# Optimization experiments

Hardware: AMD Instinct MI355X
Metric: run time of the kernel (lower is better)

Reference implementation:

```python
import jax, jax.numpy as jnp
from jax import lax
import numpy as np


def setup_inputs() -> dict:
    key = jax.random.key(0)
    ks = jax.random.split(key, 5)
    B, T, I, H, L = 64, 512, 1024, 1024, 1
    stdv = 1.0 / (H ** 0.5)
    return {
        "input": jax.random.normal(ks[0], (B, T, I), dtype=jnp.float32),
        "weight_ih": jax.random.uniform(ks[1], (L, H, I), jnp.float32, -stdv, stdv),
        "weight_hh": jax.random.uniform(ks[2], (L, H, H), jnp.float32, -stdv, stdv),
        "bias_ih": jax.random.uniform(ks[3], (L, H), jnp.float32, -stdv, stdv),
        "bias_hh": jax.random.uniform(ks[4], (L, H), jnp.float32, -stdv, stdv),
    }


def reference(input, weight_ih, weight_hh, bias_ih, bias_hh):
    # input: (B, T, I); weights per layer; hx: (L, B, H)
    L, H, I = weight_ih.shape
    B, T, _ = input.shape
    h0 = jnp.zeros((L, B, H), dtype=input.dtype)
    bias = (bias_ih + bias_hh)[:, None, :]  # (L, 1, H)
    # Hoist the input projection out of the recurrence: one big GEMM.
    x_proj = jnp.einsum("bti,lhi->tlbh", input, weight_ih)  # (T, L, B, H)

    def step(h, xp):
        # h: (L, B, H); per-layer recurrent matmul
        g = xp + jnp.einsum("lbh,lgh->lbg", h, weight_hh) + bias
        h_new = jnp.tanh(g)
        return h_new, h_new

    h_last, outs = lax.scan(step, h0, x_proj)  # outs: (T, L, B, H)
    output = jnp.transpose(outs, (1, 0, 2, 3))  # (L, T, B, H) matching torch cat(dim=1)
    return output, h_last
```

## Files before the change

kernel.cpp:

```cpp
#include <hip/hip_runtime.h>
#include <hip/hip_bf16.h>
#include <stdint.h>

#define B_ 64
#define T_ 512
#define I_ 1024
#define H_ 1024
#define BH (B_*H_)

typedef __attribute__((ext_vector_type(8))) short short8;
typedef __attribute__((ext_vector_type(4))) float f32x4;
typedef __attribute__((ext_vector_type(4))) unsigned u32x4;
typedef __attribute__((ext_vector_type(2))) unsigned u32x2;

static __device__ __forceinline__ unsigned short f2bf(float f) {
  union { float f; unsigned u; } v; v.f = f;
  unsigned r = v.u + 0x7fffu + ((v.u >> 16) & 1u);
  return (unsigned short)(r >> 16);
}

static __device__ __forceinline__ void glds16(const void* g, void* l) {
  __builtin_amdgcn_global_load_lds(
      (const __attribute__((address_space(1))) unsigned int*)g,
      (__attribute__((address_space(3))) unsigned int*)l, 16, 0, 0);
}

__global__ void convert_weights(const f32x4* __restrict__ wih, const f32x4* __restrict__ whh,
                                uint2* __restrict__ wih_b, uint2* __restrict__ whh_b)
{
  int idx = blockIdx.x * blockDim.x + threadIdx.x;
  f32x4 a = wih[idx];
  uint2 o;
  o.x = f2bf(a[0]) | ((unsigned)f2bf(a[1]) << 16);
  o.y = f2bf(a[2]) | ((unsigned)f2bf(a[3]) << 16);
  wih_b[idx] = o;
  f32x4 b = whh[idx];
  uint2 p;
  p.x = f2bf(b[0]) | ((unsigned)f2bf(b[1]) << 16);
  p.y = f2bf(b[2]) | ((unsigned)f2bf(b[3]) << 16);
  whh_b[idx] = p;
}

__global__ void convert_input(const float* __restrict__ in, unsigned short* __restrict__ inb)
{
  size_t idx = (size_t)blockIdx.x * 256 + threadIdx.x;
  size_t base = idx * 8;
  size_t R = base >> 10;
  int i = (int)(base & 1023);
  int b = (int)(R & 63), t = (int)(R >> 6);
  const float* src = in + ((size_t)b * T_ + (size_t)t) * I_ + i;
  f32x4 x0 = *(const f32x4*)src;
  f32x4 x1 = *(const f32x4*)(src + 4);
  uint4 o;
  o.x = f2bf(x0[0]) | ((unsigned)f2bf(x0[1]) << 16);
  o.y = f2bf(x0[2]) | ((unsigned)f2bf(x0[3]) << 16);
  o.z = f2bf(x1[0]) | ((unsigned)f2bf(x1[1]) << 16);
  o.w = f2bf(x1[2]) | ((unsigned)f2bf(x1[3]) << 16);
  *(uint4*)(inb + base) = o;
}

__launch_bounds__(256)
__global__ void gemm_xproj(const unsigned short* __restrict__ inb,
                           const unsigned short* __restrict__ wb,
                           const float* __restrict__ bih,
                           const float* __restrict__ bhh,
                           float* __restrict__ out)
{
  __shared__ __align__(16) unsigned char As[16384];
  __shared__ __align__(16) unsigned char Bs[16384];
  const int tid = threadIdx.x;
  const int lane = tid & 63;
  const int w = tid >> 6;
  const int wm = w >> 1, wn = w & 1;
  const int bn = blockIdx.x, bm = blockIdx.y;

  f32x4 acc[4][4];
  #pragma unroll
  for (int i = 0; i < 4; ++i)
    #pragma unroll
    for (int j = 0; j < 4; ++j)
      acc[i][j] = (f32x4){0.f,0.f,0.f,0.f};

  for (int kt = 0; kt < 16; ++kt) {
    __syncthreads();
    #pragma unroll
    for (int q = 0; q < 4; ++q) {
      int inst = w*4 + q;
      int rr = inst*8 + (lane >> 3);
      int soA = ((bm*128 + rr) * I_ + kt*64) * 2 + (((lane & 7) * 16) ^ ((rr & 7) << 4));
      int soB = ((bn*128 + rr) * I_ + kt*64) * 2 + (((lane & 7) * 16) ^ ((rr & 7) << 4));
      glds16((const unsigned char*)inb + soA, As + inst*1024);
      glds16((const unsigned char*)wb  + soB, Bs + inst*1024);
    }
    __syncthreads();
    #pragma unroll
    for (int kb = 0; kb < 2; ++kb) {
      const int kby = kb*64 + ((lane >> 4) << 4);
      short8 af[4], bfr[4];
      #pragma unroll
      for (int i = 0; i < 4; ++i) {
        int ra = wm*64 + i*16 + (lane & 15);
        af[i] = *(const short8*)(As + ra*128 + (kby ^ ((ra & 7) << 4)));
      }
      #pragma unroll
      for (int j = 0; j < 4; ++j) {
        int rb2 = wn*64 + j*16 + (lane & 15);
        bfr[j] = *(const short8*)(Bs + rb2*128 + (kby ^ ((rb2 & 7) << 4)));
      }
      #pragma unroll
      for (int i = 0; i < 4; ++i)
        #pragma unroll
        for (int j = 0; j < 4; ++j)
          acc[i][j] = __builtin_amdgcn_mfma_f32_16x16x32_bf16(af[i], bfr[j], acc[i][j], 0, 0, 0);
    }
  }
  #pragma unroll
  for (int j = 0; j < 4; ++j) {
    int col = bn*128 + wn*64 + j*16 + (lane & 15);
    float bias = bih[col] + bhh[col];
    #pragma unroll
    for (int i = 0; i < 4; ++i) {
      int Rb = bm*128 + wm*64 + i*16 + ((lane >> 4) << 2);
      #pragma unroll
      for (int q = 0; q < 4; ++q) {
        int R = Rb + q;
        out[(size_t)(R >> 6) * BH + (size_t)(R & 63) * H_ + col] = acc[i][j][q] + bias;
      }
    }
  }
}

__launch_bounds__(256, 1)
__global__ void rnn_recur(const unsigned short* __restrict__ whh_b,
                          float* __restrict__ out,
                          unsigned char* __restrict__ hx)
{
  extern __shared__ __align__(16) unsigned char lds[];
  const int tid = threadIdx.x;
  const int lane = tid & 63;
  const int w = tid >> 6;
  const int g = blockIdx.x;
  const int gb = g >> 4;
  const int gn = g & 15;

  for (int q = 0; q < 32; ++q) {
    int inst = w*32 + q;
    int nl = inst >> 1;
    int koff = (inst & 1)*1024 + lane*16;
    size_t srcoff = (size_t)(gn*64 + nl)*2048 + (size_t)(koff ^ ((nl & 7) << 4));
    glds16((const unsigned char*)whh_b + srcoff, lds + inst*1024);
  }
  asm volatile("s_waitcnt vmcnt(0)" ::: "memory");
  __syncthreads();

  const int arow = w*16 + (lane & 15);
  const unsigned char* wsrow = lds + (size_t)arow*2048;
  const int aswz = (arow & 7) << 4;
  const int klane = (lane >> 4) << 4;
  short8 af[32];
  #pragma unroll
  for (int kb = 0; kb < 32; ++kb)
    af[kb] = *(const short8*)(wsrow + ((kb*64 + klane) ^ aswz));
  __syncthreads();

  const int bb = lane & 15;
  const int nq = (lane >> 4) << 2;
  const int colb = gn*64 + w*16 + nq;
  const int brow = gb*16 + bb;
  const int bswz = (bb & 7) << 4;

  const int srow = tid & 15;
  const int scol = tid >> 4;
  const int sswz = (srow & 7) << 4;

  f32x4 xp = *(const f32x4*)(out + (size_t)brow*H_ + colb);

  for (int t = 0; t < T_; ++t) {
    unsigned char* hsb = lds + (size_t)(t & 1)*32768;
    unsigned char* sdst = hsb + srow*2048;
    if (t == 0) {
      u32x2 z = (u32x2){0u, 0u};
      #pragma unroll
      for (int j = 0; j < 16; ++j)
        *(u32x2*)(sdst + (((j*16 + scol)*8) ^ sswz)) = z;
    } else {
      const unsigned want = (unsigned)t;
      const unsigned char* pb = hx + (size_t)(t & 1)*262144 + (size_t)gb*65536 + (size_t)tid*16;
      u32x4 v0,v1,v2,v3,v4,v5,v6,v7,v8,v9,v10,v11,v12,v13,v14,v15;
      __builtin_amdgcn_s_sleep(8);
      asm volatile(
        "global_load_dwordx4 %0, %8, off sc0 sc1\n\t"
        "global_load_dwordx4 %1, %9, off sc0 sc1\n\t"
        "global_load_dwordx4 %2, %10, off sc0 sc1\n\t"
        "global_load_dwordx4 %3, %11, off sc0 sc1\n\t"
        "global_load_dwordx4 %4, %12, off sc0 sc1\n\t"
        "global_load_dwordx4 %5, %13, off sc0 sc1\n\t"
        "global_load_dwordx4 %6, %14, off sc0 sc1\n\t"
        "global_load_dwordx4 %7, %15, off sc0 sc1"
        : "=&v"(v0),"=&v"(v1),"=&v"(v2),"=&v"(v3),"=&v"(v4),"=&v"(v5),"=&v"(v6),"=&v"(v7)
        : "v"(pb), "v"(pb+4096), "v"(pb+2*4096), "v"(pb+3*4096),
          "v"(pb+4*4096), "v"(pb+5*4096), "v"(pb+6*4096), "v"(pb+7*4096)
        : "memory");
      asm volatile(
        "global_load_dwordx4 %0, %8, off sc0 sc1\n\t"
        "global_load_dwordx4 %1, %9, off sc0 sc1\n\t"
        "global_load_dwordx4 %2, %10, off sc0 sc1\n\t"
        "global_load_dwordx4 %3, %11, off sc0 sc1\n\t"
        "global_load_dwordx4 %4, %12, off sc0 sc1\n\t"
        "global_load_dwordx4 %5, %13, off sc0 sc1\n\t"
        "global_load_dwordx4 %6, %14, off sc0 sc1\n\t"
        "global_load_dwordx4 %7, %15, off sc0 sc1"
        : "=&v"(v8),"=&v"(v9),"=&v"(v10),"=&v"(v11),"=&v"(v12),"=&v"(v13),"=&v"(v14),"=&v"(v15)
        : "v"(pb+8*4096), "v"(pb+9*4096), "v"(pb+10*4096), "v"(pb+11*4096),
          "v"(pb+12*4096), "v"(pb+13*4096), "v"(pb+14*4096), "v"(pb+15*4096)
        : "memory");
      asm volatile("s_waitcnt vmcnt(0)"
        : "+v"(v0),"+v"(v1),"+v"(v2),"+v"(v3),"+v"(v4),"+v"(v5),"+v"(v6),"+v"(v7),
          "+v"(v8),"+v"(v9),"+v"(v10),"+v"(v11),"+v"(v12),"+v"(v13),"+v"(v14),"+v"(v15)
        :: "memory");
      unsigned m;
      #define MKMASK() { m = 0; \
        m |= (v0[2]==want)  ? 1u<<0  : 0u;  m |= (v1[2]==want)  ? 1u<<1  : 0u; \
        m |= (v2[2]==want)  ? 1u<<2  : 0u;  m |= (v3[2]==want)  ? 1u<<3  : 0u; \
        m |= (v4[2]==want)  ? 1u<<4  : 0u;  m |= (v5[2]==want)  ? 1u<<5  : 0u; \
        m |= (v6[2]==want)  ? 1u<<6  : 0u;  m |= (v7[2]==want)  ? 1u<<7  : 0u; \
        m |= (v8[2]==want)  ? 1u<<8  : 0u;  m |= (v9[2]==want)  ? 1u<<9  : 0u; \
        m |= (v10[2]==want) ? 1u<<10 : 0u;  m |= (v11[2]==want) ? 1u<<11 : 0u; \
        m |= (v12[2]==want) ? 1u<<12 : 0u;  m |= (v13[2]==want) ? 1u<<13 : 0u; \
        m |= (v14[2]==want) ? 1u<<14 : 0u;  m |= (v15[2]==want) ? 1u<<15 : 0u; }
      MKMASK()
      while (m != 0xffffu) {
        __builtin_amdgcn_s_sleep(1);
        #define RLD(vv, jj) if (!((m >> (jj)) & 1u)) \
          asm volatile("global_load_dwordx4 %0, %1, off sc0 sc1" \
                       : "=&v"(vv) : "v"(pb + (jj)*4096) : "memory");
        RLD(v0,0)  RLD(v1,1)  RLD(v2,2)  RLD(v3,3)
        RLD(v4,4)  RLD(v5,5)  RLD(v6,6)  RLD(v7,7)
        RLD(v8,8)  RLD(v9,9)  RLD(v10,10) RLD(v11,11)
        RLD(v12,12) RLD(v13,13) RLD(v14,14) RLD(v15,15)
        #undef RLD
        asm volatile("s_waitcnt vmcnt(0)"
          : "+v"(v0),"+v"(v1),"+v"(v2),"+v"(v3),"+v"(v4),"+v"(v5),"+v"(v6),"+v"(v7),
            "+v"(v8),"+v"(v9),"+v"(v10),"+v"(v11),"+v"(v12),"+v"(v13),"+v"(v14),"+v"(v15)
          :: "memory");
        MKMASK()
      }
      #undef MKMASK
      #define STG(vv, jj) \
        *(u32x2*)(sdst + ((((jj)*16 + scol)*8) ^ sswz)) = (u32x2){vv[0], vv[1]};
      STG(v0,0)  STG(v1,1)  STG(v2,2)  STG(v3,3)
      STG(v4,4)  STG(v5,5)  STG(v6,6)  STG(v7,7)
      STG(v8,8)  STG(v9,9)  STG(v10,10) STG(v11,11)
      STG(v12,12) STG(v13,13) STG(v14,14) STG(v15,15)
      #undef STG
    }
    asm volatile("s_waitcnt lgkmcnt(0)\n\ts_barrier" ::: "memory");

    const unsigned char* hfrow = hsb + (size_t)bb*2048;
    f32x4 acc0 = (f32x4){0.f,0.f,0.f,0.f}, acc1 = acc0, acc2 = acc0, acc3 = acc0;
    #pragma unroll
    for (int kb = 0; kb < 32; kb += 4) {
      short8 b0 = *(const short8*)(hfrow + ((kb*64 + klane) ^ bswz));
      short8 b1 = *(const short8*)(hfrow + (((kb+1)*64 + klane) ^ bswz));
      short8 b2 = *(const short8*)(hfrow + (((kb+2)*64 + klane) ^ bswz));
      short8 b3 = *(const short8*)(hfrow + (((kb+3)*64 + klane) ^ bswz));
      acc0 = __builtin_amdgcn_mfma_f32_16x16x32_bf16(af[kb],   b0, acc0, 0, 0, 0);
      acc1 = __builtin_amdgcn_mfma_f32_16x16x32_bf16(af[kb+1], b1, acc1, 0, 0, 0);
      acc2 = __builtin_amdgcn_mfma_f32_16x16x32_bf16(af[kb+2], b2, acc2, 0, 0, 0);
      acc3 = __builtin_amdgcn_mfma_f32_16x16x32_bf16(af[kb+3], b3, acc3, 0, 0, 0);
    }
    f32x4 hval;
    #pragma unroll
    for (int q = 0; q < 4; ++q)
      hval[q] = tanhf((acc0[q] + acc1[q]) + (acc2[q] + acc3[q]) + xp[q]);

    u32x4 pkt;
    pkt[0] = f2bf(hval[0]) | ((unsigned)f2bf(hval[1]) << 16);
    pkt[1] = f2bf(hval[2]) | ((unsigned)f2bf(hval[3]) << 16);
    pkt[2] = (unsigned)(t + 1);
    pkt[3] = 0u;
    const unsigned char* wp = hx + (size_t)((t+1) & 1)*262144 + (size_t)gb*65536
                              + (size_t)(gn*256 + tid)*16;
    asm volatile("global_store_dwordx4 %0, %1, off sc0 sc1" :: "v"(wp), "v"(pkt) : "memory");

    *(f32x4*)(out + (size_t)t*BH + (size_t)brow*H_ + colb) = hval;
    if (t == T_-1)
      *(f32x4*)(out + (size_t)T_*BH + (size_t)brow*H_ + colb) = hval;

    int tn = (t < T_-1) ? t+1 : t;
    xp = *(const f32x4*)(out + (size_t)tn*BH + (size_t)brow*H_ + colb);
  }
}

extern "C" void kernel_launch(void* const* d_in, const int* in_sizes, int n_in,
                              void* d_out, int out_size, void* d_ws, size_t ws_size,
                              hipStream_t stream)
{
  const float* in  = (const float*)d_in[0];
  const float* wih = (const float*)d_in[1];
  const float* whh = (const float*)d_in[2];
  const float* bih = (const float*)d_in[3];
  const float* bhh = (const float*)d_in[4];
  float* out = (float*)d_out;
  unsigned char* ws = (unsigned char*)d_ws;

  unsigned char*  hx    = ws;
  unsigned short* wih_b = (unsigned short*)(ws + 524288);
  unsigned short* whh_b = (unsigned short*)(ws + 524288 + 2097152);
  unsigned short* inb   = (unsigned short*)(ws + 524288 + 4194304);

  hipMemsetAsync(hx, 0, 524288, stream);
  convert_weights<<<1024, 256, 0, stream>>>((const f32x4*)wih, (const f32x4*)whh,
                                            (uint2*)wih_b, (uint2*)whh_b);
  convert_input<<<16384, 256, 0, stream>>>(in, inb);
  gemm_xproj<<<dim3(8, 256), 256, 0, stream>>>(inb, whh_b == 0 ? 0 : wih_b, bih, bhh, out);
  rnn_recur<<<64, 256, 131072, stream>>>(whh_b, out, hx);
}
```

Baseline: 1.556 ms.

## Fuse input-projection GEMM with recurrence using per-row-block completion flags

Merges the fp32-to-bf16 input conversion into the GEMM's A-tile loader and runs the GEMM and the recurrence in a single launch. The first 64 blocks do the recurrence and the other 2048 blocks compute x_proj tiles. Each GEMM tile bumps an atomic flag per row-block, and a recurrent step spins on that flag before it reads x_proj, so the recurrence can start before the whole GEMM finishes. This removes a separate conversion pass and the kernel boundary. The risks are that the persistent recurrent blocks must be resident alongside the GEMM blocks, which a 128KB LDS request per block may limit, and that the x_proj reads now go uncached through sc0 sc1 loads.

```diff
diff --git a/kernel.cpp b/kernel.cpp
--- a/kernel.cpp
+++ b/kernel.cpp
@@ -41,104 +41,115 @@
   whh_b[idx] = p;
 }
 
-__global__ void convert_input(const float* __restrict__ in, unsigned short* __restrict__ inb)
+__launch_bounds__(256, 1)
+__global__ void fused_gemm_rnn(const float* __restrict__ in,
+                               const unsigned short* __restrict__ wih_b,
+                               const unsigned short* __restrict__ whh_b,
+                               const float* __restrict__ bih,
+                               const float* __restrict__ bhh,
+                               float* __restrict__ out,
+                               unsigned char* __restrict__ hx)
 {
-  size_t idx = (size_t)blockIdx.x * 256 + threadIdx.x;
-  size_t base = idx * 8;
-  size_t R = base >> 10;
-  int i = (int)(base & 1023);
-  int b = (int)(R & 63), t = (int)(R >> 6);
-  const float* src = in + ((size_t)b * T_ + (size_t)t) * I_ + i;
-  f32x4 x0 = *(const f32x4*)src;
-  f32x4 x1 = *(const f32x4*)(src + 4);
-  uint4 o;
-  o.x = f2bf(x0[0]) | ((unsigned)f2bf(x0[1]) << 16);
-  o.y = f2bf(x0[2]) | ((unsigned)f2bf(x0[3]) << 16);
-  o.z = f2bf(x1[0]) | ((unsigned)f2bf(x1[1]) << 16);
-  o.w = f2bf(x1[2]) | ((unsigned)f2bf(x1[3]) << 16);
-  *(uint4*)(inb + base) = o;
-}
-
-__launch_bounds__(256)
-__global__ void gemm_xproj(const unsigned short* __restrict__ inb,
-                           const unsigned short* __restrict__ wb,
-                           const float* __restrict__ bih,
-                           const float* __restrict__ bhh,
-                           float* __restrict__ out)
-{
-  __shared__ __align__(16) unsigned char As[16384];
-  __shared__ __align__(16) unsigned char Bs[16384];
+  extern __shared__ __align__(16) unsigned char lds[];
+  unsigned* flags = (unsigned*)(hx + 524288);
   const int tid = threadIdx.x;
   const int lane = tid & 63;
   const int w = tid >> 6;
-  const int wm = w >> 1, wn = w & 1;
-  const int bn = blockIdx.x, bm = blockIdx.y;
-
-  f32x4 acc[4][4];
-  #pragma unroll
-  for (int i = 0; i < 4; ++i)
-    #pragma unroll
-    for (int j = 0; j < 4; ++j)
-      acc[i][j] = (f32x4){0.f,0.f,0.f,0.f};
-
-  for (int kt = 0; kt < 16; ++kt) {
+
+  if (blockIdx.x >= 64) {
+    const int idx = blockIdx.x - 64;
+    const int bn = idx & 7;
+    const int bm = idx >> 3;
+    unsigned char* As = lds;
+    unsigned char* Bs = lds + 16384;
+    const int wm_ = w >> 1, wn = w & 1;
+
+    const int ar = tid >> 1;
+    const int ah = tid & 1;
+    const int R0 = bm*128 + ar;
+    const float* asrc = in + (size_t)(R0 & 63) * (T_*I_) + (size_t)(R0 >> 6) * I_ + ah*32;
+    unsigned char* adst_base = As + ar*128;
+    const int aswz_w = (ar & 7) << 4;
+
+    f32x4 acc[4][4];
+    #pragma unroll
+    for (int i = 0; i < 4; ++i)
+      #pragma unroll
+      for (int j = 0; j < 4; ++j)
+        acc[i][j] = (f32x4){0.f,0.f,0.f,0.f};
+
+    f32x4 av[8];
+    #pragma unroll
+    for (int j = 0; j < 8; ++j) av[j] = *(const f32x4*)(asrc + 0*64 + j*4);
+
+    for (int kt = 0; kt < 16; ++kt) {
+      __syncthreads();
+      #pragma unroll
+      for (int q = 0; q < 4; ++q) {
+        int inst = w*4 + q;
+        int rb = inst*8 + (lane >> 3);
+        int srcoff = ((bn*128 + rb) * I_ + kt*64) * 2 + (((lane & 7) * 16) ^ ((rb & 7) << 4));
+        glds16((const unsigned char*)wih_b + srcoff, Bs + inst*1024);
+      }
+      #pragma unroll
+      for (int j2 = 0; j2 < 4; ++j2) {
+        uint4 val;
+        f32x4 v0 = av[j2*2], v1 = av[j2*2+1];
+        val.x = f2bf(v0[0]) | ((unsigned)f2bf(v0[1]) << 16);
+        val.y = f2bf(v0[2]) | ((unsigned)f2bf(v0[3]) << 16);
+        val.z = f2bf(v1[0]) | ((unsigned)f2bf(v1[1]) << 16);
+        val.w = f2bf(v1[2]) | ((unsigned)f2bf(v1[3]) << 16);
+        int koffb = ah*64 + j2*16;
+        *(uint4*)(adst_base + (koffb ^ aswz_w)) = val;
+      }
+      __syncthreads();
+      if (kt < 15) {
+        #pragma unroll
+        for (int j = 0; j < 8; ++j) av[j] = *(const f32x4*)(asrc + (kt+1)*64 + j*4);
+      }
+      #pragma unroll
+      for (int kb = 0; kb < 2; ++kb) {
+        const int kby = kb*64 + ((lane >> 4) << 4);
+        short8 af2[4], bfr[4];
+        #pragma unroll
+        for (int i = 0; i < 4; ++i) {
+          int ra = wm_*64 + i*16 + (lane & 15);
+          af2[i] = *(const short8*)(As + ra*128 + (kby ^ ((ra & 7) << 4)));
+        }
+        #pragma unroll
+        for (int j = 0; j < 4; ++j) {
+          int rb2 = wn*64 + j*16 + (lane & 15);
+          bfr[j] = *(const short8*)(Bs + rb2*128 + (kby ^ ((rb2 & 7) << 4)));
+        }
+        #pragma unroll
+        for (int i = 0; i < 4; ++i)
+          #pragma unroll
+          for (int j = 0; j < 4; ++j)
+            acc[i][j] = __builtin_amdgcn_mfma_f32_16x16x32_bf16(af2[i], bfr[j], acc[i][j], 0, 0, 0);
+      }
+    }
+    #pragma unroll
+    for (int j = 0; j < 4; ++j) {
+      int col = bn*128 + wn*64 + j*16 + (lane & 15);
+      float bias = bih[col] + bhh[col];
+      #pragma unroll
+      for (int i = 0; i < 4; ++i) {
+        int Rb = bm*128 + wm_*64 + i*16 + ((lane >> 4) << 2);
+        #pragma unroll
+        for (int q = 0; q < 4; ++q) {
+          int R = Rb + q;
+          float vv = acc[i][j][q] + bias;
+          const float* addr = out + (size_t)(R >> 6) * BH + (size_t)(R & 63) * H_ + col;
+          asm volatile("global_store_dword %0, %1, off sc0 sc1" :: "v"(addr), "v"(vv) : "memory");
+        }
+      }
+    }
+    asm volatile("s_waitcnt vmcnt(0)" ::: "memory");
     __syncthreads();
-    #pragma unroll
-    for (int q = 0; q < 4; ++q) {
-      int inst = w*4 + q;
-      int rr = inst*8 + (lane >> 3);
-      int soA = ((bm*128 + rr) * I_ + kt*64) * 2 + (((lane & 7) * 16) ^ ((rr & 7) << 4));
-      int soB = ((bn*128 + rr) * I_ + kt*64) * 2 + (((lane & 7) * 16) ^ ((rr & 7) << 4));
-      glds16((const unsigned char*)inb + soA, As + inst*1024);
-      glds16((const unsigned char*)wb  + soB, Bs + inst*1024);
-    }
-    __syncthreads();
-    #pragma unroll
-    for (int kb = 0; kb < 2; ++kb) {
-      const int kby = kb*64 + ((lane >> 4) << 4);
-      short8 af[4], bfr[4];
-      #pragma unroll
-      for (int i = 0; i < 4; ++i) {
-        int ra = wm*64 + i*16 + (lane & 15);
-        af[i] = *(const short8*)(As + ra*128 + (kby ^ ((ra & 7) << 4)));
-      }
-      #pragma unroll
-      for (int j = 0; j < 4; ++j) {
-        int rb2 = wn*64 + j*16 + (lane & 15);
-        bfr[j] = *(const short8*)(Bs + rb2*128 + (kby ^ ((rb2 & 7) << 4)));
-      }
-      #pragma unroll
-      for (int i = 0; i < 4; ++i)
-        #pragma unroll
-        for (int j = 0; j < 4; ++j)
-          acc[i][j] = __builtin_amdgcn_mfma_f32_16x16x32_bf16(af[i], bfr[j], acc[i][j], 0, 0, 0);
-    }
+    if (tid == 0) atomicAdd(flags + bm, 1u);
+    return;
   }
-  #pragma unroll
-  for (int j = 0; j < 4; ++j) {
-    int col = bn*128 + wn*64 + j*16 + (lane & 15);
-    float bias = bih[col] + bhh[col];
-    #pragma unroll
-    for (int i = 0; i < 4; ++i) {
-      int Rb = bm*128 + wm*64 + i*16 + ((lane >> 4) << 2);
-      #pragma unroll
-      for (int q = 0; q < 4; ++q) {
-        int R = Rb + q;
-        out[(size_t)(R >> 6) * BH + (size_t)(R & 63) * H_ + col] = acc[i][j][q] + bias;
-      }
-    }
-  }
-}
-
-__launch_bounds__(256, 1)
-__global__ void rnn_recur(const unsigned short* __restrict__ whh_b,
-                          float* __restrict__ out,
-                          unsigned char* __restrict__ hx)
-{
-  extern __shared__ __align__(16) unsigned char lds[];
-  const int tid = threadIdx.x;
-  const int lane = tid & 63;
-  const int w = tid >> 6;
+
   const int g = blockIdx.x;
   const int gb = g >> 4;
   const int gn = g & 15;
@@ -173,9 +184,17 @@
   const int scol = tid >> 4;
   const int sswz = (srow & 7) << 4;
 
-  f32x4 xp = *(const f32x4*)(out + (size_t)brow*H_ + colb);
+  int wmk = 0;
+  f32x4 xp;
 
   for (int t = 0; t < T_; ++t) {
+    const int bmt = t >> 1;
+    while (wmk <= bmt) {
+      unsigned f = __hip_atomic_load(flags + wmk, __ATOMIC_RELAXED, __HIP_MEMORY_SCOPE_AGENT);
+      if (f >= 8) ++wmk; else __builtin_amdgcn_s_sleep(1);
+    }
+    const float* xpa = out + (size_t)t*BH + (size_t)brow*H_ + colb;
+
     unsigned char* hsb = lds + (size_t)(t & 1)*32768;
     unsigned char* sdst = hsb + srow*2048;
     if (t == 0) {
@@ -183,6 +202,8 @@
       #pragma unroll
       for (int j = 0; j < 16; ++j)
         *(u32x2*)(sdst + (((j*16 + scol)*8) ^ sswz)) = z;
+      asm volatile("global_load_dwordx4 %0, %1, off sc0 sc1\n\ts_waitcnt vmcnt(0)"
+                   : "=v"(xp) : "v"(xpa) : "memory");
     } else {
       const unsigned want = (unsigned)t;
       const unsigned char* pb = hx + (size_t)(t & 1)*262144 + (size_t)gb*65536 + (size_t)tid*16;
@@ -214,9 +235,11 @@
         : "v"(pb+8*4096), "v"(pb+9*4096), "v"(pb+10*4096), "v"(pb+11*4096),
           "v"(pb+12*4096), "v"(pb+13*4096), "v"(pb+14*4096), "v"(pb+15*4096)
         : "memory");
+      asm volatile("global_load_dwordx4 %0, %1, off sc0 sc1" : "=&v"(xp) : "v"(xpa) : "memory");
       asm volatile("s_waitcnt vmcnt(0)"
         : "+v"(v0),"+v"(v1),"+v"(v2),"+v"(v3),"+v"(v4),"+v"(v5),"+v"(v6),"+v"(v7),
-          "+v"(v8),"+v"(v9),"+v"(v10),"+v"(v11),"+v"(v12),"+v"(v13),"+v"(v14),"+v"(v15)
+          "+v"(v8),"+v"(v9),"+v"(v10),"+v"(v11),"+v"(v12),"+v"(v13),"+v"(v14),"+v"(v15),
+          "+v"(xp)
         :: "memory");
       unsigned m;
       #define MKMASK() { m = 0; \
@@ -286,9 +309,6 @@
     *(f32x4*)(out + (size_t)t*BH + (size_t)brow*H_ + colb) = hval;
     if (t == T_-1)
       *(f32x4*)(out + (size_t)T_*BH + (size_t)brow*H_ + colb) = hval;
-
-    int tn = (t < T_-1) ? t+1 : t;
-    xp = *(const f32x4*)(out + (size_t)tn*BH + (size_t)brow*H_ + colb);
   }
 }
 
@@ -305,14 +325,11 @@
   unsigned char* ws = (unsigned char*)d_ws;
 
   unsigned char*  hx    = ws;
-  unsigned short* wih_b = (unsigned short*)(ws + 524288);
-  unsigned short* whh_b = (unsigned short*)(ws + 524288 + 2097152);
-  unsigned short* inb   = (unsigned short*)(ws + 524288 + 4194304);
-
-  hipMemsetAsync(hx, 0, 524288, stream);
+  unsigned short* wih_b = (unsigned short*)(ws + 532480);
+  unsigned short* whh_b = (unsigned short*)(ws + 532480 + 2097152);
+
+  hipMemsetAsync(hx, 0, 532480, stream);
   convert_weights<<<1024, 256, 0, stream>>>((const f32x4*)wih, (const f32x4*)whh,
                                             (uint2*)wih_b, (uint2*)whh_b);
-  convert_input<<<16384, 256, 0, stream>>>(in, inb);
-  gemm_xproj<<<dim3(8, 256), 256, 0, stream>>>(inb, whh_b == 0 ? 0 : wih_b, bih, bhh, out);
-  rnn_recur<<<64, 256, 131072, stream>>>(whh_b, out, hx);
-}
+  fused_gemm_rnn<<<2112, 256, 131072, stream>>>(in, wih_b, whh_b, bih, bhh, out, hx);
+}
```

Measured after the change: 1.574 ms. Within noise of the previous version (+1.1%).

## Halve recurrent workgroups to 32 with 512 threads covering 128 hidden columns each

Applied to the files above, without the earlier changes.

Reorganises the persistent recurrence kernel from 64 workgroups of 256 threads (64 columns each) to 32 workgroups of 512 threads (128 columns each), loading the W_hh slice into registers in two LDS rounds. Each workgroup now polls half as many 16-byte packets per step from the global h exchange buffer, with the packet layout remapped to match. The aim is to reduce the number of cross-workgroup synchronisation participants and the per-step polling traffic. In exchange, each CU runs 8 waves with 32 A-fragment registers each, and only 32 CUs are used.

```diff
diff --git a/kernel.cpp b/kernel.cpp
--- a/kernel.cpp
+++ b/kernel.cpp
@@ -130,7 +130,7 @@
   }
 }
 
-__launch_bounds__(256, 1)
+__launch_bounds__(512, 2)
 __global__ void rnn_recur(const unsigned short* __restrict__ whh_b,
                           float* __restrict__ out,
                           unsigned char* __restrict__ hx)
@@ -138,40 +138,48 @@
   extern __shared__ __align__(16) unsigned char lds[];
   const int tid = threadIdx.x;
   const int lane = tid & 63;
-  const int w = tid >> 6;
+  const int wv = tid >> 6;
   const int g = blockIdx.x;
-  const int gb = g >> 4;
-  const int gn = g & 15;
-
-  for (int q = 0; q < 32; ++q) {
-    int inst = w*32 + q;
-    int nl = inst >> 1;
-    int koff = (inst & 1)*1024 + lane*16;
-    size_t srcoff = (size_t)(gn*64 + nl)*2048 + (size_t)(koff ^ ((nl & 7) << 4));
-    glds16((const unsigned char*)whh_b + srcoff, lds + inst*1024);
+  const int gb = g >> 3;
+  const int gq = g & 7;
+
+  short8 af[32];
+  const int wvr = wv & 3;
+  const int arow_s = wvr*16 + (lane & 15);
+  const unsigned char* wsrow = lds + (size_t)arow_s*2048;
+  const int aswz = (arow_s & 7) << 4;
+  const int klane = (lane >> 4) << 4;
+  #pragma unroll
+  for (int r = 0; r < 2; ++r) {
+    #pragma unroll
+    for (int q = 0; q < 16; ++q) {
+      int inst = wv*16 + q;
+      int nl = inst >> 1;
+      int koff = (inst & 1)*1024 + lane*16;
+      size_t srcoff = (size_t)(gq*128 + r*64 + nl)*2048 + (size_t)(koff ^ ((nl & 7) << 4));
+      glds16((const unsigned char*)whh_b + srcoff, lds + inst*1024);
+    }
+    asm volatile("s_waitcnt vmcnt(0)" ::: "memory");
+    __syncthreads();
+    if ((wv >> 2) == r) {
+      #pragma unroll
+      for (int kb = 0; kb < 32; ++kb)
+        af[kb] = *(const short8*)(wsrow + ((kb*64 + klane) ^ aswz));
+    }
+    __syncthreads();
   }
-  asm volatile("s_waitcnt vmcnt(0)" ::: "memory");
-  __syncthreads();
-
-  const int arow = w*16 + (lane & 15);
-  const unsigned char* wsrow = lds + (size_t)arow*2048;
-  const int aswz = (arow & 7) << 4;
-  const int klane = (lane >> 4) << 4;
-  short8 af[32];
-  #pragma unroll
-  for (int kb = 0; kb < 32; ++kb)
-    af[kb] = *(const short8*)(wsrow + ((kb*64 + klane) ^ aswz));
-  __syncthreads();
 
   const int bb = lane & 15;
   const int nq = (lane >> 4) << 2;
-  const int colb = gn*64 + w*16 + nq;
+  const int colb = gq*128 + wv*16 + nq;
   const int brow = gb*16 + bb;
   const int bswz = (bb & 7) << 4;
 
   const int srow = tid & 15;
-  const int scol = tid >> 4;
+  const int scb = (tid >> 4) * 8;
   const int sswz = (srow & 7) << 4;
+
+  const int pp = (gq*32 + wv*4 + (nq >> 2))*16 + bb;
 
   f32x4 xp = *(const f32x4*)(out + (size_t)brow*H_ + colb);
 
@@ -181,12 +189,12 @@
     if (t == 0) {
       u32x2 z = (u32x2){0u, 0u};
       #pragma unroll
-      for (int j = 0; j < 16; ++j)
-        *(u32x2*)(sdst + (((j*16 + scol)*8) ^ sswz)) = z;
+      for (int j = 0; j < 8; ++j)
+        *(u32x2*)(sdst + ((j*256 + scb) ^ sswz)) = z;
     } else {
       const unsigned want = (unsigned)t;
       const unsigned char* pb = hx + (size_t)(t & 1)*262144 + (size_t)gb*65536 + (size_t)tid*16;
-      u32x4 v0,v1,v2,v3,v4,v5,v6,v7,v8,v9,v10,v11,v12,v13,v14,v15;
+      u32x4 v0,v1,v2,v3,v4,v5,v6,v7;
       __builtin_amdgcn_s_sleep(8);
       asm volatile(
         "global_load_dwordx4 %0, %8, off sc0 sc1\n\t"
@@ -198,60 +206,37 @@
         "global_load_dwordx4 %6, %14, off sc0 sc1\n\t"
         "global_load_dwordx4 %7, %15, off sc0 sc1"
         : "=&v"(v0),"=&v"(v1),"=&v"(v2),"=&v"(v3),"=&v"(v4),"=&v"(v5),"=&v"(v6),"=&v"(v7)
-        : "v"(pb), "v"(pb+4096), "v"(pb+2*4096), "v"(pb+3*4096),
-          "v"(pb+4*4096), "v"(pb+5*4096), "v"(pb+6*4096), "v"(pb+7*4096)
-        : "memory");
-      asm volatile(
-        "global_load_dwordx4 %0, %8, off sc0 sc1\n\t"
-        "global_load_dwordx4 %1, %9, off sc0 sc1\n\t"
-        "global_load_dwordx4 %2, %10, off sc0 sc1\n\t"
-        "global_load_dwordx4 %3, %11, off sc0 sc1\n\t"
-        "global_load_dwordx4 %4, %12, off sc0 sc1\n\t"
-        "global_load_dwordx4 %5, %13, off sc0 sc1\n\t"
-        "global_load_dwordx4 %6, %14, off sc0 sc1\n\t"
-        "global_load_dwordx4 %7, %15, off sc0 sc1"
-        : "=&v"(v8),"=&v"(v9),"=&v"(v10),"=&v"(v11),"=&v"(v12),"=&v"(v13),"=&v"(v14),"=&v"(v15)
-        : "v"(pb+8*4096), "v"(pb+9*4096), "v"(pb+10*4096), "v"(pb+11*4096),
-          "v"(pb+12*4096), "v"(pb+13*4096), "v"(pb+14*4096), "v"(pb+15*4096)
+        : "v"(pb), "v"(pb+8192), "v"(pb+2*8192), "v"(pb+3*8192),
+          "v"(pb+4*8192), "v"(pb+5*8192), "v"(pb+6*8192), "v"(pb+7*8192)
         : "memory");
       asm volatile("s_waitcnt vmcnt(0)"
-        : "+v"(v0),"+v"(v1),"+v"(v2),"+v"(v3),"+v"(v4),"+v"(v5),"+v"(v6),"+v"(v7),
-          "+v"(v8),"+v"(v9),"+v"(v10),"+v"(v11),"+v"(v12),"+v"(v13),"+v"(v14),"+v"(v15)
+        : "+v"(v0),"+v"(v1),"+v"(v2),"+v"(v3),"+v"(v4),"+v"(v5),"+v"(v6),"+v"(v7)
         :: "memory");
       unsigned m;
       #define MKMASK() { m = 0; \
-        m |= (v0[2]==want)  ? 1u<<0  : 0u;  m |= (v1[2]==want)  ? 1u<<1  : 0u; \
-        m |= (v2[2]==want)  ? 1u<<2  : 0u;  m |= (v3[2]==want)  ? 1u<<3  : 0u; \
-        m |= (v4[2]==want)  ? 1u<<4  : 0u;  m |= (v5[2]==want)  ? 1u<<5  : 0u; \
-        m |= (v6[2]==want)  ? 1u<<6  : 0u;  m |= (v7[2]==want)  ? 1u<<7  : 0u; \
-        m |= (v8[2]==want)  ? 1u<<8  : 0u;  m |= (v9[2]==want)  ? 1u<<9  : 0u; \
-        m |= (v10[2]==want) ? 1u<<10 : 0u;  m |= (v11[2]==want) ? 1u<<11 : 0u; \
-        m |= (v12[2]==want) ? 1u<<12 : 0u;  m |= (v13[2]==want) ? 1u<<13 : 0u; \
-        m |= (v14[2]==want) ? 1u<<14 : 0u;  m |= (v15[2]==want) ? 1u<<15 : 0u; }
+        m |= (v0[2]==want) ? 1u<<0 : 0u;  m |= (v1[2]==want) ? 1u<<1 : 0u; \
+        m |= (v2[2]==want) ? 1u<<2 : 0u;  m |= (v3[2]==want) ? 1u<<3 : 0u; \
+        m |= (v4[2]==want) ? 1u<<4 : 0u;  m |= (v5[2]==want) ? 1u<<5 : 0u; \
+        m |= (v6[2]==want) ? 1u<<6 : 0u;  m |= (v7[2]==want) ? 1u<<7 : 0u; }
       MKMASK()
-      while (m != 0xffffu) {
+      while (m != 0xffu) {
         __builtin_amdgcn_s_sleep(1);
         #define RLD(vv, jj) if (!((m >> (jj)) & 1u)) \
           asm volatile("global_load_dwordx4 %0, %1, off sc0 sc1" \
-                       : "=&v"(vv) : "v"(pb + (jj)*4096) : "memory");
-        RLD(v0,0)  RLD(v1,1)  RLD(v2,2)  RLD(v3,3)
-        RLD(v4,4)  RLD(v5,5)  RLD(v6,6)  RLD(v7,7)
-        RLD(v8,8)  RLD(v9,9)  RLD(v10,10) RLD(v11,11)
-        RLD(v12,12) RLD(v13,13) RLD(v14,14) RLD(v15,15)
+                       : "=&v"(vv) : "v"(pb + (jj)*8192) : "memory");
+        RLD(v0,0) RLD(v1,1) RLD(v2,2) RLD(v3,3)
+        RLD(v4,4) RLD(v5,5) RLD(v6,6) RLD(v7,7)
         #undef RLD
         asm volatile("s_waitcnt vmcnt(0)"
-          : "+v"(v0),"+v"(v1),"+v"(v2),"+v"(v3),"+v"(v4),"+v"(v5),"+v"(v6),"+v"(v7),
-            "+v"(v8),"+v"(v9),"+v"(v10),"+v"(v11),"+v"(v12),"+v"(v13),"+v"(v14),"+v"(v15)
+          : "+v"(v0),"+v"(v1),"+v"(v2),"+v"(v3),"+v"(v4),"+v"(v5),"+v"(v6),"+v"(v7)
           :: "memory");
         MKMASK()
       }
       #undef MKMASK
       #define STG(vv, jj) \
-        *(u32x2*)(sdst + ((((jj)*16 + scol)*8) ^ sswz)) = (u32x2){vv[0], vv[1]};
-      STG(v0,0)  STG(v1,1)  STG(v2,2)  STG(v3,3)
-      STG(v4,4)  STG(v5,5)  STG(v6,6)  STG(v7,7)
-      STG(v8,8)  STG(v9,9)  STG(v10,10) STG(v11,11)
-      STG(v12,12) STG(v13,13) STG(v14,14) STG(v15,15)
+        *(u32x2*)(sdst + (((jj)*256 + scb) ^ sswz)) = (u32x2){vv[0], vv[1]};
+      STG(v0,0) STG(v1,1) STG(v2,2) STG(v3,3)
+      STG(v4,4) STG(v5,5) STG(v6,6) STG(v7,7)
       #undef STG
     }
     asm volatile("s_waitcnt lgkmcnt(0)\n\ts_barrier" ::: "memory");
@@ -280,7 +265,7 @@
     pkt[2] = (unsigned)(t + 1);
     pkt[3] = 0u;
     const unsigned char* wp = hx + (size_t)((t+1) & 1)*262144 + (size_t)gb*65536
-                              + (size_t)(gn*256 + tid)*16;
+                              + (size_t)pp*16;
     asm volatile("global_store_dwordx4 %0, %1, off sc0 sc1" :: "v"(wp), "v"(pkt) : "memory");
 
     *(f32x4*)(out + (size_t)t*BH + (size_t)brow*H_ + colb) = hval;
@@ -313,6 +298,6 @@
   convert_weights<<<1024, 256, 0, stream>>>((const f32x4*)wih, (const f32x4*)whh,
                                             (uint2*)wih_b, (uint2*)whh_b);
   convert_input<<<16384, 256, 0, stream>>>(in, inb);
-  gemm_xproj<<<dim3(8, 256), 256, 0, stream>>>(inb, whh_b == 0 ? 0 : wih_b, bih, bhh, out);
-  rnn_recur<<<64, 256, 131072, stream>>>(whh_b, out, hx);
-}
+  gemm_xproj<<<dim3(8, 256), 256, 0, stream>>>(inb, wih_b, bih, bhh, out);
+  rnn_recur<<<32, 512, 131072, stream>>>(whh_b, out, hx);
+}
```

New measurement: 1.688 ms. +8.5%, slower.
